# Performance work log

Hardware: AMD Instinct MI355X
Metric: run time of the kernel (lower is better)

## Reference

```python
import jax, jax.numpy as jnp
import numpy as np

B, D_IN, D_OUT = 8192, 4096, 4096
IN_DIMS = (64, 64)
OUT_DIMS = (64, 64)
# tt_rank_rate=0.5 over dims [64,64,64,64] -> ranks [1,32,1024,32,1]
RANKS = (1, 32, 1024, 32, 1)


def _kaiming_uniform(key, shape):
    # matches nn.init.kaiming_uniform_(a=sqrt(5)) on a (r_prev, d, r) tensor:
    # fan_in = prod(shape[1:]) = d * r, gain = sqrt(2/(1+5)) = sqrt(1/3)
    fan_in = shape[1] * shape[2]
    bound = np.sqrt(1.0 / 3.0) * np.sqrt(3.0 / fan_in)
    return jax.random.uniform(key, shape, jnp.float32, -bound, bound)


def setup_inputs() -> dict:
    key = jax.random.key(0)
    kx, k0, k1, k2, k3, kb = jax.random.split(key, 6)
    dims = list(IN_DIMS) + list(OUT_DIMS)
    shapes = [(RANKS[i], dims[i], RANKS[i + 1]) for i in range(4)]
    x = jax.random.normal(kx, (B, D_IN), jnp.float32)
    core0 = _kaiming_uniform(k0, shapes[0])  # (1, 64, 32)
    core1 = _kaiming_uniform(k1, shapes[1])  # (32, 64, 1024)
    core2 = _kaiming_uniform(k2, shapes[2])  # (1024, 64, 32)
    core3 = _kaiming_uniform(k3, shapes[3])  # (32, 64, 1)
    bb = 1.0 / np.sqrt(D_IN)
    bias = jax.random.uniform(kb, (D_OUT,), jnp.float32, -bb, bb)
    return {"x": x, "core0": core0, "core1": core1, "core2": core2,
            "core3": core3, "bias": bias}


def reference(x, core0, core1, core2, core3, bias):
    b = x.shape[0]
    s = x.reshape(b, IN_DIMS[0], IN_DIMS[1])          # (B, 64, 64)
    # input core 0: contract first input dim (rank-in = 1 squeezed)
    s = jnp.einsum('bcd,cs->bds', s, core0[0])        # (B, 64, 32)
    # input core 1: contract second input dim and rank
    s = jnp.einsum('bcr,rcs->bs', s, core1)           # (B, 1024)
    # output core 2: expand first output dim
    s = jnp.einsum('br,rAs->bAs', s, core2)           # (B, 64, 32)
    # output core 3: expand second output dim (rank-out = 1 squeezed)
    s = jnp.einsum('bAr,rB->bAB', s, core3[..., 0])   # (B, 64, 64)
    return s.reshape(b, -1) + bias                    # (B, 4096)
```

## Files before the change

### kernel.cpp

```cpp
#include <hip/hip_runtime.h>
#include <hip/hip_bf16.h>


typedef _Float16 h4 __attribute__((ext_vector_type(4)));
typedef _Float16 h8 __attribute__((ext_vector_type(8)));
typedef float f32x4 __attribute__((ext_vector_type(4)));

#define BATCH 8192

__device__ __forceinline__ void gld_lds16(const void* g, void* l) {
  __builtin_amdgcn_global_load_lds(
      (__attribute__((address_space(1))) void*)(g),
      (__attribute__((address_space(3))) void*)(l), 16, 0, 0);
}

__global__ __launch_bounds__(256) void transpose_cast2(
    const float* __restrict__ c1, _Float16* __restrict__ W1t,
    const float* __restrict__ c2, _Float16* __restrict__ W2t) {
  __shared__ float t[64][65];
  const int which = blockIdx.z;
  const float* src = which ? c2 : c1;
  _Float16* dst = which ? W2t : W1t;
  const int K = which ? 1024 : 2048, U = which ? 2048 : 1024;
  const int k0 = (which ? blockIdx.y : blockIdx.x) * 64;
  const int u0 = (which ? blockIdx.x : blockIdx.y) * 64;
  const int tx = threadIdx.x & 63, ty = threadIdx.x >> 6;
  for (int i = ty; i < 64; i += 4) {
    const int k = k0 + i;
    const int sr = which ? k : ((k & 31) * 64 + (k >> 5));
    t[i][tx] = src[(size_t)sr * U + u0 + tx];
  }
  __syncthreads();
  for (int i = ty; i < 64; i += 4) {
    dst[(size_t)(u0 + i) * K + k0 + tx] = (_Float16)t[tx][i];
  }
}

__global__ __launch_bounds__(256) void stage2(const float* __restrict__ x,
                                              const float* __restrict__ c0,
                                              _Float16* __restrict__ s1) {
  __shared__ _Float16 xh[4 * 4096];
  __shared__ float c0l[2048];
  const int b0 = blockIdx.x * 4;
  const int tid = threadIdx.x;

  {
    const float4* xg = (const float4*)(x + (size_t)b0 * 4096);
#pragma unroll
    for (int k = 0; k < 16; ++k) {
      float4 v = xg[tid + 256 * k];
      h4 w = {(_Float16)v.x, (_Float16)v.y, (_Float16)v.z, (_Float16)v.w};
      ((h4*)xh)[tid + 256 * k] = w;
    }
    ((float4*)c0l)[tid] = ((const float4*)c0)[tid];
    ((float4*)c0l)[tid + 256] = ((const float4*)c0)[tid + 256];
  }
  __syncthreads();

  const int row = tid >> 6, t6 = tid & 63;
  const int d0 = (t6 >> 3) * 8;
  const int r0 = (t6 & 7) * 4;
  const _Float16* xrow = xh + row * 4096;

  float acc[8][4];
#pragma unroll
  for (int i = 0; i < 8; ++i)
#pragma unroll
    for (int j = 0; j < 4; ++j) acc[i][j] = 0.0f;

  for (int c = 0; c < 64; ++c) {
    h8 xv = *(const h8*)&xrow[c * 64 + d0];
    f32x4 wv = *(const f32x4*)&c0l[c * 32 + r0];
#pragma unroll
    for (int i = 0; i < 8; ++i) {
      const float xf = (float)xv[i];
#pragma unroll
      for (int j = 0; j < 4; ++j) acc[i][j] += xf * wv[j];
    }
  }

  _Float16* s1row = s1 + (size_t)(b0 + row) * 2048;
#pragma unroll
  for (int i = 0; i < 8; ++i) {
    h4 o = {(_Float16)acc[i][0], (_Float16)acc[i][1], (_Float16)acc[i][2],
            (_Float16)acc[i][3]};
    *(h4*)&s1row[(d0 + i) * 32 + r0] = o;
  }
}

template <int K, int CN>
__global__ __launch_bounds__(512, 2) void gemm_pipe(
    const _Float16* __restrict__ A, const _Float16* __restrict__ Bt,
    _Float16* __restrict__ C) {
  __shared__ __align__(16) char lds[3 * 49152];
  constexpr int NT = K / 64;
  const int bm = blockIdx.x, bn = blockIdx.y;
  const int tid = threadIdx.x;
  const int w = tid >> 6, lane = tid & 63;
  const int lr = lane & 15, kh = lane >> 4;
  const int wmo = (w >> 2) << 6, wno = (w & 3) << 6;

  f32x4 acc[4][4] = {};

  const int sr = tid >> 3;
  const int sc = ((tid & 7) ^ (sr & 7)) << 4;
  const char* gA = (const char*)(A + (size_t)(bm * 128 + sr) * K) + sc;
  const char* gB = (const char*)(Bt + (size_t)(bn * 256 + sr) * K) + sc;
  const size_t rk = (size_t)K * 128;
  char* lw = lds + (w << 10);

  auto STAGE_A = [&](int t) {
    char* b_ = lw + (t % 3) * 49152;
    const char* ga = gA + (size_t)t * 128;
    gld_lds16(ga, b_);
    gld_lds16(ga + rk, b_ + 8192);
    gld_lds16(gB + (size_t)t * 128, b_ + 16384);
  };
  auto STAGE_B = [&](int t) {
    char* b_ = lw + (t % 3) * 49152;
    const char* gb = gB + (size_t)t * 128;
    gld_lds16(gb + rk, b_ + 24576);
    gld_lds16(gb + 2 * rk, b_ + 32768);
    gld_lds16(gb + 3 * rk, b_ + 40960);
  };

  auto KTILE = [&](int t, bool last) {
    if (last)
      asm volatile("s_waitcnt vmcnt(0)" ::: "memory");
    else
      asm volatile("s_waitcnt vmcnt(6)" ::: "memory");
    __builtin_amdgcn_s_barrier();
    __builtin_amdgcn_sched_barrier(0);
    const char* bufA = lds + (t % 3) * 49152;
    const char* bufB = bufA + 16384;
    h8 af[2][4], bf[2][4];
#pragma unroll
    for (int kk = 0; kk < 2; ++kk) {
#pragma unroll
      for (int m = 0; m < 4; ++m) {
        const int R = wmo + m * 16 + lr;
        af[kk][m] = *(const h8*)(bufA + R * 128 +
                                 ((((kk << 2) + kh) ^ (R & 7)) << 4));
      }
#pragma unroll
      for (int n = 0; n < 2; ++n) {
        const int R = wno + n * 16 + lr;
        bf[kk][n] = *(const h8*)(bufB + R * 128 +
                                 ((((kk << 2) + kh) ^ (R & 7)) << 4));
      }
    }
    if (t + 2 < NT) STAGE_A(t + 2);
    asm volatile("s_waitcnt lgkmcnt(0)" ::: "memory");
    __builtin_amdgcn_sched_barrier(0);
    __builtin_amdgcn_s_setprio(1);
#pragma unroll
    for (int kk = 0; kk < 2; ++kk)
#pragma unroll
      for (int m = 0; m < 4; ++m)
#pragma unroll
        for (int n = 0; n < 2; ++n)
          acc[m][n] = __builtin_amdgcn_mfma_f32_16x16x32_f16(
              af[kk][m], bf[kk][n], acc[m][n], 0, 0, 0);
    __builtin_amdgcn_s_setprio(0);
    __builtin_amdgcn_s_barrier();
    __builtin_amdgcn_sched_barrier(0);
#pragma unroll
    for (int kk = 0; kk < 2; ++kk)
#pragma unroll
      for (int n = 2; n < 4; ++n) {
        const int R = wno + n * 16 + lr;
        bf[kk][n] = *(const h8*)(bufB + R * 128 +
                                 ((((kk << 2) + kh) ^ (R & 7)) << 4));
      }
    if (t + 2 < NT) STAGE_B(t + 2);
    asm volatile("s_waitcnt lgkmcnt(0)" ::: "memory");
    __builtin_amdgcn_sched_barrier(0);
    __builtin_amdgcn_s_setprio(1);
#pragma unroll
    for (int kk = 0; kk < 2; ++kk)
#pragma unroll
      for (int m = 0; m < 4; ++m)
#pragma unroll
        for (int n = 2; n < 4; ++n)
          acc[m][n] = __builtin_amdgcn_mfma_f32_16x16x32_f16(
              af[kk][m], bf[kk][n], acc[m][n], 0, 0, 0);
    __builtin_amdgcn_s_setprio(0);
  };

  STAGE_A(0); STAGE_B(0);
  STAGE_A(1); STAGE_B(1);
  for (int t = 0; t < NT - 1; ++t) KTILE(t, false);
  KTILE(NT - 1, true);

#pragma unroll
  for (int m = 0; m < 4; ++m) {
    const int r0 = bm * 128 + wmo + m * 16 + kh * 4;
#pragma unroll
    for (int n = 0; n < 4; ++n) {
      const int c0 = bn * 256 + wno + n * 16 + lr;
#pragma unroll
      for (int q = 0; q < 4; ++q)
        C[(size_t)(r0 + q) * CN + c0] = (_Float16)acc[m][n][q];
    }
  }
}

template <int K>
__global__ __launch_bounds__(512, 2) void gemm2_8ph(
    const _Float16* __restrict__ A, const _Float16* __restrict__ Bt,
    const float* __restrict__ c3, const float* __restrict__ bias,
    float* __restrict__ out) {
  __shared__ __align__(16) char lds[131072];
  constexpr int NT = K / 64;
  const int bm = blockIdx.x, bn = blockIdx.y;
  const int tid = threadIdx.x;
  const int w = tid >> 6, lane = tid & 63;
  const int lr = lane & 15, kh = lane >> 4;
  const int l7 = lr & 7;

  f32x4 acc[8][4] = {};

  const int sr = tid >> 3;
  const int sc = ((tid & 7) ^ (sr & 7)) << 4;
  const size_t rowK = (size_t)K * 2;
  const char* gA = (const char*)A + (size_t)(bm * 256 + sr) * rowK + sc;
  const char* gB = (const char*)Bt + (size_t)(bn * 256 + sr) * rowK + sc;
  char* lw = lds + (w << 10);

  auto STAGE = [&](int kind, int t) {
    char* d = lw + kind * 32768 + (t & 1) * 16384;
    const char* g = (kind < 2 ? gA : gB) + (size_t)(kind & 1) * 128 * rowK +
                    (size_t)t * 128;
    gld_lds16(g, d);
    gld_lds16(g + 64 * rowK, d + 8192);
  };

  const char* bufA0 = lds + (w >> 2) * 32768;
  const char* bufB0 = lds + 65536 + ((w & 3) >> 1) * 32768;
  const int bcol = (w & 1) * 64;

  h8 af[2][4], bflo[2][2], bfhi[2][2];

  STAGE(0, 0); STAGE(1, 0); STAGE(2, 0); STAGE(3, 0);
  STAGE(2, 1); STAGE(0, 1); STAGE(1, 1);
  asm volatile("s_waitcnt vmcnt(6)" ::: "memory");
  __builtin_amdgcn_sched_barrier(0);
  __builtin_amdgcn_s_barrier();

  for (int t = 0; t < NT; ++t) {
    const char* bA = bufA0 + (t & 1) * 16384;
    const char* bB = bufB0 + (t & 1) * 16384;
#pragma unroll
    for (int kk = 0; kk < 2; ++kk) {
#pragma unroll
      for (int m = 0; m < 4; ++m)
        af[kk][m] = *(const h8*)(bA + (m * 16 + lr) * 128 +
                                 ((((kk << 2) + kh) ^ l7) << 4));
#pragma unroll
      for (int n = 0; n < 2; ++n)
        bflo[kk][n] = *(const h8*)(bB + (bcol + n * 16 + lr) * 128 +
                                   ((((kk << 2) + kh) ^ l7) << 4));
    }
    if (t + 1 < NT) STAGE(3, t + 1);
    __builtin_amdgcn_sched_barrier(0);
    __builtin_amdgcn_s_barrier();
    asm volatile("s_waitcnt lgkmcnt(0)" ::: "memory");
    __builtin_amdgcn_sched_barrier(0);
    __builtin_amdgcn_s_setprio(1);
#pragma unroll
    for (int kk = 0; kk < 2; ++kk)
#pragma unroll
      for (int m = 0; m < 4; ++m)
#pragma unroll
        for (int n = 0; n < 2; ++n)
          acc[m][n] = __builtin_amdgcn_mfma_f32_16x16x32_f16(
              af[kk][m], bflo[kk][n], acc[m][n], 0, 0, 0);
    __builtin_amdgcn_s_setprio(0);
    __builtin_amdgcn_s_barrier();
#pragma unroll
    for (int kk = 0; kk < 2; ++kk)
#pragma unroll
      for (int n = 0; n < 2; ++n)
        bfhi[kk][n] = *(const h8*)(bB + (bcol + 32 + n * 16 + lr) * 128 +
                                   ((((kk << 2) + kh) ^ l7) << 4));
    if (t + 2 < NT) STAGE(2, t + 2);
    __builtin_amdgcn_sched_barrier(0);
    __builtin_amdgcn_s_barrier();
    asm volatile("s_waitcnt lgkmcnt(0)" ::: "memory");
    __builtin_amdgcn_sched_barrier(0);
    __builtin_amdgcn_s_setprio(1);
#pragma unroll
    for (int kk = 0; kk < 2; ++kk)
#pragma unroll
      for (int m = 0; m < 4; ++m)
#pragma unroll
        for (int n = 0; n < 2; ++n)
          acc[m][2 + n] = __builtin_amdgcn_mfma_f32_16x16x32_f16(
              af[kk][m], bfhi[kk][n], acc[m][2 + n], 0, 0, 0);
    __builtin_amdgcn_s_setprio(0);
    __builtin_amdgcn_s_barrier();
#pragma unroll
    for (int kk = 0; kk < 2; ++kk)
#pragma unroll
      for (int m = 0; m < 4; ++m)
        af[kk][m] = *(const h8*)(bA + (64 + m * 16 + lr) * 128 +
                                 ((((kk << 2) + kh) ^ l7) << 4));
    __builtin_amdgcn_sched_barrier(0);
    __builtin_amdgcn_s_barrier();
    asm volatile("s_waitcnt lgkmcnt(0)" ::: "memory");
    __builtin_amdgcn_sched_barrier(0);
    __builtin_amdgcn_s_setprio(1);
#pragma unroll
    for (int kk = 0; kk < 2; ++kk)
#pragma unroll
      for (int m = 0; m < 4; ++m)
#pragma unroll
        for (int n = 0; n < 2; ++n)
          acc[4 + m][n] = __builtin_amdgcn_mfma_f32_16x16x32_f16(
              af[kk][m], bflo[kk][n], acc[4 + m][n], 0, 0, 0);
    __builtin_amdgcn_s_setprio(0);
    __builtin_amdgcn_s_barrier();
    if (t + 2 < NT) { STAGE(0, t + 2); STAGE(1, t + 2); }
    __builtin_amdgcn_sched_barrier(0);
    __builtin_amdgcn_s_barrier();
    __builtin_amdgcn_s_setprio(1);
#pragma unroll
    for (int kk = 0; kk < 2; ++kk)
#pragma unroll
      for (int m = 0; m < 4; ++m)
#pragma unroll
        for (int n = 0; n < 2; ++n)
          acc[4 + m][2 + n] = __builtin_amdgcn_mfma_f32_16x16x32_f16(
              af[kk][m], bfhi[kk][n], acc[4 + m][2 + n], 0, 0, 0);
    __builtin_amdgcn_s_setprio(0);
    if (t + 2 < NT)
      asm volatile("s_waitcnt vmcnt(6)" ::: "memory");
    else
      asm volatile("s_waitcnt vmcnt(0)" ::: "memory");
    __builtin_amdgcn_sched_barrier(0);
    __builtin_amdgcn_s_barrier();
  }

  h8 bfe[4];
  float bb[8][4];
#pragma unroll
  for (int n = 0; n < 4; ++n) {
#pragma unroll
    for (int j = 0; j < 8; ++j)
      bfe[n][j] = (_Float16)c3[(kh * 8 + j) * 64 + n * 16 + lr];
#pragma unroll
    for (int a = 0; a < 8; ++a)
      bb[a][n] = bias[(bn * 8 + a) * 64 + n * 16 + lr];
  }
  __syncthreads();
  {
    const int wmo = (w >> 2) << 7;
    const int wno = (w & 3) << 6;
#pragma unroll
    for (int m = 0; m < 8; ++m) {
      const int Rb = wmo + m * 16 + kh * 4;
#pragma unroll
      for (int n = 0; n < 4; ++n) {
        const int cc = wno + n * 16 + lr;
#pragma unroll
        for (int q = 0; q < 4; ++q) {
          const int R = Rb + q;
          *(_Float16*)(lds + R * 512 +
                       ((((cc >> 3) ^ (R & 7)) << 4) | ((cc & 7) << 1))) =
              (_Float16)acc[m][n][q];
        }
      }
    }
  }
  __syncthreads();
  const int r32 = w << 5;
#pragma unroll
  for (int mi = 0; mi < 2; ++mi) {
    const int rr = r32 + mi * 16 + lr;
    const int orow0 = bm * 256 + r32 + mi * 16 + (kh << 2);
#pragma unroll
    for (int a = 0; a < 8; ++a) {
      h8 afv = *(const h8*)(lds + rr * 512 +
                            ((((a * 4 + kh) ^ (rr & 7)) << 4)));
#pragma unroll
      for (int n = 0; n < 4; ++n) {
        f32x4 d = {};
        d = __builtin_amdgcn_mfma_f32_16x16x32_f16(afv, bfe[n], d, 0, 0, 0);
        const int ocol = (bn * 8 + a) * 64 + n * 16 + lr;
#pragma unroll
        for (int q = 0; q < 4; ++q)
          out[(size_t)(orow0 + q) * 4096 + ocol] = d[q] + bb[a][n];
      }
    }
  }
}

extern "C" void kernel_launch(void* const* d_in, const int* in_sizes, int n_in,
                              void* d_out, int out_size, void* d_ws,
                              size_t ws_size, hipStream_t stream) {
  (void)in_sizes; (void)n_in; (void)out_size; (void)ws_size;
  const float* x     = (const float*)d_in[0];
  const float* core0 = (const float*)d_in[1];
  const float* core1 = (const float*)d_in[2];
  const float* core2 = (const float*)d_in[3];
  const float* core3 = (const float*)d_in[4];
  const float* bias  = (const float*)d_in[5];
  float* out = (float*)d_out;

  char* ws = (char*)d_ws;
  _Float16* s1h = (_Float16*)ws;
  _Float16* s2h = (_Float16*)(ws + 33554432);
  _Float16* W1t = (_Float16*)(ws + 50331648);
  _Float16* W2t = (_Float16*)(ws + 54525952);

  transpose_cast2<<<dim3(32, 16, 2), 256, 0, stream>>>(core1, W1t, core2, W2t);
  stage2<<<BATCH / 4, 256, 0, stream>>>(x, core0, s1h);
  gemm_pipe<2048, 1024><<<dim3(BATCH / 128, 4), 512, 0, stream>>>(s1h, W1t, s2h);
  gemm2_8ph<1024><<<dim3(BATCH / 256, 2048 / 256), 512, 0, stream>>>(
      s2h, W2t, core3, bias, out);
}
```

Measured before the change: 149.1 us.

## Use fdot2 in stage2 and write epilogue output as vectorized rows

The first-stage contraction now converts x and core0 into paired-half layouts in LDS and accumulates with packed fp16 dot products instead of scalar fp32 FMAs. The final GEMM epilogue swaps the MFMA operands so each lane owns four contiguous output columns. That lets it preload bias as the accumulator and store 16-byte float4 vectors instead of strided scalar stores. This is meant to cut ALU work in stage2 and improve coalescing of the large fp32 output write, at the cost of slightly different rounding behaviour in the fdot2 path.

```diff
diff --git a/kernel.cpp b/kernel.cpp
--- a/kernel.cpp
+++ b/kernel.cpp
@@ -2,11 +2,20 @@
 #include <hip/hip_bf16.h>
 
 
+typedef _Float16 h2 __attribute__((ext_vector_type(2)));
 typedef _Float16 h4 __attribute__((ext_vector_type(4)));
 typedef _Float16 h8 __attribute__((ext_vector_type(8)));
 typedef float f32x4 __attribute__((ext_vector_type(4)));
 
 #define BATCH 8192
+
+#if __has_builtin(__builtin_amdgcn_fdot2)
+#define FDOT2(a, b, c) __builtin_amdgcn_fdot2((a), (b), (c), false)
+#else
+__device__ __forceinline__ float FDOT2(h2 a, h2 b, float c) {
+  return c + (float)a[0] * (float)b[0] + (float)a[1] * (float)b[1];
+}
+#endif
 
 __device__ __forceinline__ void gld_lds16(const void* g, void* l) {
   __builtin_amdgcn_global_load_lds(
@@ -39,43 +48,55 @@
 __global__ __launch_bounds__(256) void stage2(const float* __restrict__ x,
                                               const float* __restrict__ c0,
                                               _Float16* __restrict__ s1) {
-  __shared__ _Float16 xh[4 * 4096];
-  __shared__ float c0l[2048];
+  __shared__ _Float16 xh2[4 * 4096];
+  __shared__ _Float16 c0h[2048];
   const int b0 = blockIdx.x * 4;
   const int tid = threadIdx.x;
 
   {
-    const float4* xg = (const float4*)(x + (size_t)b0 * 4096);
-#pragma unroll
-    for (int k = 0; k < 16; ++k) {
-      float4 v = xg[tid + 256 * k];
-      h4 w = {(_Float16)v.x, (_Float16)v.y, (_Float16)v.z, (_Float16)v.w};
-      ((h4*)xh)[tid + 256 * k] = w;
-    }
-    ((float4*)c0l)[tid] = ((const float4*)c0)[tid];
-    ((float4*)c0l)[tid + 256] = ((const float4*)c0)[tid + 256];
+#pragma unroll
+    for (int i = 0; i < 8; ++i) {
+      const int flat = tid + 256 * i;
+      const int row = flat >> 9;
+      const int s = flat & 511;
+      const int cp = s >> 4, d0 = (s & 15) * 4;
+      const float* gb = x + (size_t)(b0 + row) * 4096 + cp * 128 + d0;
+      float4 fa = *(const float4*)gb;
+      float4 fb = *(const float4*)(gb + 64);
+      h8 o = {(_Float16)fa.x, (_Float16)fb.x, (_Float16)fa.y, (_Float16)fb.y,
+              (_Float16)fa.z, (_Float16)fb.z, (_Float16)fa.w, (_Float16)fb.w};
+      *(h8*)&xh2[row * 4096 + cp * 128 + d0 * 2] = o;
+    }
+#pragma unroll
+    for (int i = 0; i < 4; ++i) {
+      const int p = tid + 256 * i;
+      const int cp = p >> 5, r = p & 31;
+      h2 o = {(_Float16)c0[cp * 64 + r], (_Float16)c0[cp * 64 + 32 + r]};
+      *(h2*)&c0h[cp * 64 + r * 2] = o;
+    }
   }
   __syncthreads();
 
   const int row = tid >> 6, t6 = tid & 63;
   const int d0 = (t6 >> 3) * 8;
   const int r0 = (t6 & 7) * 4;
-  const _Float16* xrow = xh + row * 4096;
-
-  float acc[8][4];
-#pragma unroll
-  for (int i = 0; i < 8; ++i)
-#pragma unroll
-    for (int j = 0; j < 4; ++j) acc[i][j] = 0.0f;
-
-  for (int c = 0; c < 64; ++c) {
-    h8 xv = *(const h8*)&xrow[c * 64 + d0];
-    f32x4 wv = *(const f32x4*)&c0l[c * 32 + r0];
-#pragma unroll
-    for (int i = 0; i < 8; ++i) {
-      const float xf = (float)xv[i];
-#pragma unroll
-      for (int j = 0; j < 4; ++j) acc[i][j] += xf * wv[j];
+  const _Float16* xrow = xh2 + row * 4096;
+
+  float acc[8][4] = {};
+  for (int cp = 0; cp < 32; ++cp) {
+    h8 xa = *(const h8*)&xrow[cp * 128 + d0 * 2];
+    h8 xb = *(const h8*)&xrow[cp * 128 + d0 * 2 + 8];
+    h8 wv = *(const h8*)&c0h[cp * 64 + r0 * 2];
+#pragma unroll
+    for (int i = 0; i < 4; ++i) {
+      h2 xi = {xa[2 * i], xa[2 * i + 1]};
+      h2 xj = {xb[2 * i], xb[2 * i + 1]};
+#pragma unroll
+      for (int j = 0; j < 4; ++j) {
+        h2 wj = {wv[2 * j], wv[2 * j + 1]};
+        acc[i][j] = FDOT2(xi, wj, acc[i][j]);
+        acc[i + 4][j] = FDOT2(xj, wj, acc[i + 4][j]);
+      }
     }
   }
 
@@ -342,16 +363,11 @@
   }
 
   h8 bfe[4];
-  float bb[8][4];
-#pragma unroll
-  for (int n = 0; n < 4; ++n) {
+#pragma unroll
+  for (int n = 0; n < 4; ++n)
 #pragma unroll
     for (int j = 0; j < 8; ++j)
       bfe[n][j] = (_Float16)c3[(kh * 8 + j) * 64 + n * 16 + lr];
-#pragma unroll
-    for (int a = 0; a < 8; ++a)
-      bb[a][n] = bias[(bn * 8 + a) * 64 + n * 16 + lr];
-  }
   __syncthreads();
   {
     const int wmo = (w >> 2) << 7;
@@ -375,21 +391,22 @@
   __syncthreads();
   const int r32 = w << 5;
 #pragma unroll
-  for (int mi = 0; mi < 2; ++mi) {
-    const int rr = r32 + mi * 16 + lr;
-    const int orow0 = bm * 256 + r32 + mi * 16 + (kh << 2);
-#pragma unroll
-    for (int a = 0; a < 8; ++a) {
+  for (int a = 0; a < 8; ++a) {
+    f32x4 bs[4];
+#pragma unroll
+    for (int n = 0; n < 4; ++n)
+      bs[n] = *(const f32x4*)&bias[(bn * 8 + a) * 64 + n * 16 + kh * 4];
+#pragma unroll
+    for (int mi = 0; mi < 2; ++mi) {
+      const int rr = r32 + mi * 16 + lr;
       h8 afv = *(const h8*)(lds + rr * 512 +
                             ((((a * 4 + kh) ^ (rr & 7)) << 4)));
+      const size_t orow = (size_t)(bm * 256 + r32 + mi * 16 + lr);
 #pragma unroll
       for (int n = 0; n < 4; ++n) {
-        f32x4 d = {};
-        d = __builtin_amdgcn_mfma_f32_16x16x32_f16(afv, bfe[n], d, 0, 0, 0);
-        const int ocol = (bn * 8 + a) * 64 + n * 16 + lr;
-#pragma unroll
-        for (int q = 0; q < 4; ++q)
-          out[(size_t)(orow0 + q) * 4096 + ocol] = d[q] + bb[a][n];
+        f32x4 d = __builtin_amdgcn_mfma_f32_16x16x32_f16(bfe[n], afv, bs[n],
+                                                         0, 0, 0);
+        *(f32x4*)&out[orow * 4096 + (bn * 8 + a) * 64 + n * 16 + kh * 4] = d;
       }
     }
   }
```

New measurement: 148.8 us, median of 2. About the same (-0.2%).
